# Kernel tuning notes

Measured on AMD Instinct MI355X. Metric: run time of the kernel, lower is better.

The kernel has to match this reference:

```python
import jax, jax.numpy as jnp
import numpy as np

B, S, D = 2, 2048, 2048
H, KV, HD = 32, 8, 64          # n_heads, n_kv_heads, head_dim
NREP = H // KV                 # GQA repeat factor
ROPE_THETA = 500000.0          # llama3 base


def setup_inputs() -> dict:
    key = jax.random.key(0)
    ks = jax.random.split(key, 5)
    scale = 1.0 / np.sqrt(D)
    x = jax.random.normal(ks[0], (B, S, D), dtype=jnp.float32)
    wq = jax.random.normal(ks[1], (D, H * HD), dtype=jnp.float32) * scale
    wk = jax.random.normal(ks[2], (D, KV * HD), dtype=jnp.float32) * scale
    wv = jax.random.normal(ks[3], (D, KV * HD), dtype=jnp.float32) * scale
    wo = jax.random.normal(ks[4], (H * HD, D), dtype=jnp.float32) * scale
    # real rotary freqs, matching precompute_freqs_cis: angle[t, j] = t / theta^(2j/HD)
    inv_freq = 1.0 / (ROPE_THETA ** (np.arange(0, HD, 2, dtype=np.float32) / HD))
    t = np.arange(S, dtype=np.float32)
    ang = np.outer(t, inv_freq)  # (S, HD//2)
    freqs_cos = jnp.asarray(np.cos(ang), dtype=jnp.float32)
    freqs_sin = jnp.asarray(np.sin(ang), dtype=jnp.float32)
    return {"x": x, "wq": wq, "wk": wk, "wv": wv, "wo": wo,
            "freqs_cos": freqs_cos, "freqs_sin": freqs_sin}


def _apply_rope(t, cos, sin):
    # t: (B, S, nh, HD); pairs (even, odd) = (real, imag) of complex number
    tr = t.reshape(*t.shape[:-1], HD // 2, 2)
    re, im = tr[..., 0], tr[..., 1]
    c = cos[None, :, None, :]   # (1, S, 1, HD//2)
    s = sin[None, :, None, :]
    out_re = re * c - im * s
    out_im = re * s + im * c
    return jnp.stack([out_re, out_im], axis=-1).reshape(t.shape)


def reference(x, wq, wk, wv, wo, freqs_cos, freqs_sin):
    bsz, seq_len, _ = x.shape
    xq = (x @ wq).reshape(bsz, seq_len, H, HD)
    xk = (x @ wk).reshape(bsz, seq_len, KV, HD)
    xv = (x @ wv).reshape(bsz, seq_len, KV, HD)
    xq = _apply_rope(xq, freqs_cos, freqs_sin)
    xk = _apply_rope(xk, freqs_cos, freqs_sin)
    # GQA without materializing repeated KV: group query heads by KV head
    q = xq.transpose(0, 2, 1, 3).reshape(bsz, KV, NREP, seq_len, HD)  # bgrqh
    k = xk.transpose(0, 2, 1, 3)                                      # bgkh over seq k
    v = xv.transpose(0, 2, 1, 3)
    scores = jnp.einsum("bgrqh,bgkh->bgrqk", q, k) / jnp.sqrt(jnp.float32(HD))
    causal = jnp.tril(jnp.ones((seq_len, seq_len), dtype=bool))
    scores = jnp.where(causal[None, None, None], scores, -jnp.inf)
    probs = jax.nn.softmax(scores.astype(jnp.float32), axis=-1).astype(q.dtype)
    out = jnp.einsum("bgrqk,bgkh->bgrqh", probs, v)
    out = out.reshape(bsz, H, seq_len, HD).transpose(0, 2, 1, 3).reshape(bsz, seq_len, H * HD)
    return out @ wo
```

## Files before the change

kernel.cpp:

```cpp
#include <hip/hip_runtime.h>
#include <hip/hip_bf16.h>

typedef __attribute__((ext_vector_type(8))) short bf16x8;
typedef __attribute__((ext_vector_type(4))) float f32x4;
typedef __attribute__((ext_vector_type(16))) float f32x16;

#define S_LEN 2048
#define DMODEL 2048
#define NH 32
#define NKV 8
#define HDIM 64
#define NQKV 3072
#define BROWS 4096
#define LOG2E 1.4426950408889634f

__device__ __forceinline__ float bf2f(unsigned short u) {
    union { unsigned int i; float f; } v; v.i = ((unsigned int)u) << 16; return v.f;
}
__device__ __forceinline__ unsigned short f2bf(float f) {
    union { float f; unsigned int i; } v; v.f = f;
    unsigned int r = v.i + 0x7fffu + ((v.i >> 16) & 1u);
    return (unsigned short)(r >> 16);
}

__device__ __forceinline__ unsigned cvtpk_bf16(float lo, float hi) {
    unsigned r;
    asm("v_cvt_pk_bf16_f32 %0, %1, %2" : "=v"(r) : "v"(lo), "v"(hi));
    return r;
}
__device__ __forceinline__ void pl32swap(unsigned &a, unsigned &b) {
    asm("v_permlane32_swap_b32 %0, %1" : "+v"(a), "+v"(b));
}
__device__ __forceinline__ float exp2_fast(float x) {
    float r;
    asm("v_exp_f32 %0, %1" : "=v"(r) : "v"(x));
    return r;
}

__device__ __forceinline__ void gload_lds16(const void* g, void* l) {
    __builtin_amdgcn_global_load_lds(
        (const __attribute__((address_space(1))) unsigned int*)(unsigned long long)g,
        (__attribute__((address_space(3))) unsigned int*)(unsigned int)(unsigned long long)l,
        16, 0, 0);
}

#define VMW(n) asm volatile("s_waitcnt vmcnt(" #n ")" ::: "memory")
#define CFENCE() asm volatile("" ::: "memory")

__global__ void cast_x_kernel(const float* __restrict__ x, unsigned short* __restrict__ xb) {
    int idx = blockIdx.x * blockDim.x + threadIdx.x;
    float4 v = ((const float4*)x)[idx];
    ushort4 o;
    o.x = f2bf(v.x); o.y = f2bf(v.y); o.z = f2bf(v.z); o.w = f2bf(v.w);
    ((ushort4*)xb)[idx] = o;
}

__global__ void tcast_kernel(const float* __restrict__ src, unsigned short* __restrict__ dst,
                             int K, int N) {
    __shared__ float t[32][33];
    int n0 = blockIdx.x * 32, k0 = blockIdx.y * 32;
    int tx = threadIdx.x & 31, ty = threadIdx.x >> 5;
#pragma unroll
    for (int i = 0; i < 32; i += 8)
        t[ty + i][tx] = src[(size_t)(k0 + ty + i) * N + n0 + tx];
    __syncthreads();
#pragma unroll
    for (int i = 0; i < 32; i += 8)
        dst[(size_t)(n0 + ty + i) * K + k0 + tx] = f2bf(t[tx][ty + i]);
}

__global__ void vtrans_kernel(const unsigned short* __restrict__ qkv,
                              unsigned short* __restrict__ vt) {
    __shared__ unsigned short t[32][33];
    int s0 = blockIdx.x * 32;
    int hd0 = (blockIdx.y & 1) * 32;
    int bg = blockIdx.y >> 1;
    int b = bg >> 3, g = bg & 7;
    int tx = threadIdx.x & 31, ty = threadIdx.x >> 5;
#pragma unroll
    for (int i = 0; i < 32; i += 8)
        t[ty + i][tx] = qkv[(size_t)(b * S_LEN + s0 + ty + i) * NQKV + 2560 + g * 64 + hd0 + tx];
    __syncthreads();
#pragma unroll
    for (int i = 0; i < 32; i += 8)
        vt[(size_t)(bg * 64 + hd0 + ty + i) * S_LEN + s0 + tx] = t[tx][ty + i];
}

template <int NJF, int OUTF32>
__global__ __launch_bounds__(512, 2) void gemm_deep_kernel(
    const unsigned short* __restrict__ A,
    const unsigned short* __restrict__ BT,
    void* __restrict__ Cv,
    int M, int N, int K, int nbx) {
    extern __shared__ __align__(16) unsigned short lds[];
    constexpr int BUFS = 4096 + NJF * 2048;
    constexpr int NBL = NJF / 2;

    const int nwg = gridDim.x;
    const int cpx = nwg >> 3;
    const int swz = ((int)blockIdx.x & 7) * cpx + ((int)blockIdx.x >> 3);
    const int m0 = (swz / nbx) * 128, n0 = (swz % nbx) * (NJF * 64);

    const int tid = threadIdx.x;
    const int lane = tid & 63, wid = tid >> 6;
    const int wr = wid >> 2, wc = wid & 3;
    const int l16 = lane & 15, lg = lane >> 4;

    const int sr = tid >> 2, sk = tid & 3;
    const int kc = (sk ^ ((sr >> 1) & 3)) * 8;
    const size_t K128 = (size_t)128 * K;
    const unsigned short* gA = A + (size_t)(m0 + sr) * K + kc;
    const unsigned short* gB = BT + (size_t)(n0 + sr) * K + kc;

#define DSTAGE(T) do { \
    const int _b = (T) & 3; \
    gload_lds16(gA + (size_t)(T) * 32, lds + _b * BUFS + tid * 8); \
    _Pragma("unroll") for (int j = 0; j < NBL; ++j) \
        gload_lds16(gB + (size_t)(T) * 32 + (size_t)j * K128, \
                    lds + _b * BUFS + 4096 + j * 4096 + tid * 8); \
} while (0)
#define VMW_3L() do { if constexpr (NJF == 6) { VMW(12); } else { VMW(9); } } while (0)
#define VMW_2L() do { if constexpr (NJF == 6) { VMW(8); } else { VMW(6); } } while (0)
#define VMW_1L() do { if constexpr (NJF == 6) { VMW(4); } else { VMW(3); } } while (0)

    f32x4 acc[4][NJF];
#pragma unroll
    for (int i = 0; i < 4; ++i)
#pragma unroll
        for (int j = 0; j < NJF; ++j)
#pragma unroll
            for (int e = 0; e < 4; ++e) acc[i][j][e] = 0.f;

    const int NT = K >> 5;
    DSTAGE(0); DSTAGE(1); DSTAGE(2);

    for (int t = 0; t < NT; ++t) {
        if (t + 3 < NT) { DSTAGE(t + 3); VMW_3L(); }
        else if (t + 2 < NT) { VMW_2L(); }
        else if (t + 1 < NT) { VMW_1L(); }
        else { VMW(0); }
        __builtin_amdgcn_s_barrier();
        CFENCE();

        const unsigned short* bufp = lds + (t & 3) * BUFS;
        bf16x8 af[4], bfv[NJF];
#pragma unroll
        for (int mi = 0; mi < 4; ++mi) {
            const int rA = wr * 64 + mi * 16 + l16;
            af[mi] = *(const bf16x8*)(bufp + rA * 32 + ((lg ^ ((rA >> 1) & 3)) * 8));
        }
#pragma unroll
        for (int nj = 0; nj < NJF; ++nj) {
            const int rB = nj * 64 + wc * 16 + l16;
            bfv[nj] = *(const bf16x8*)(bufp + 4096 + rB * 32 + ((lg ^ ((rB >> 1) & 3)) * 8));
        }
#pragma unroll
        for (int mi = 0; mi < 4; ++mi)
#pragma unroll
            for (int nj = 0; nj < NJF; ++nj)
                acc[mi][nj] = __builtin_amdgcn_mfma_f32_16x16x32_bf16(
                    af[mi], bfv[nj], acc[mi][nj], 0, 0, 0);
        CFENCE();
        __builtin_amdgcn_s_barrier();
        CFENCE();
    }

#pragma unroll
    for (int mi = 0; mi < 4; ++mi) {
        const int row = m0 + wr * 64 + mi * 16 + lg * 4;
#pragma unroll
        for (int e = 0; e < 4; ++e) {
            if (OUTF32) {
                float* Cf = (float*)Cv;
#pragma unroll
                for (int nj = 0; nj < NJF; ++nj)
                    Cf[(size_t)(row + e) * N + n0 + nj * 64 + wc * 16 + l16] = acc[mi][nj][e];
            } else {
                unsigned short* Cb = (unsigned short*)Cv;
#pragma unroll
                for (int nj = 0; nj < NJF; ++nj)
                    Cb[(size_t)(row + e) * N + n0 + nj * 64 + wc * 16 + l16] = f2bf(acc[mi][nj][e]);
            }
        }
    }
#undef DSTAGE
#undef VMW_3L
#undef VMW_2L
#undef VMW_1L
}

template <int OUTF32>
__global__ __launch_bounds__(256) void gemm_bt_kernel(
    const unsigned short* __restrict__ A,
    const unsigned short* __restrict__ BT,
    void* __restrict__ Cv,
    int M, int N, int K) {
    __shared__ __align__(16) unsigned short Als[128 * 32];
    __shared__ __align__(16) unsigned short Bls[128 * 32];

    const int tid = threadIdx.x;
    const int lane = tid & 63;
    const int wid = tid >> 6;
    const int wr = wid >> 1, wc = wid & 1;
    const int l16 = lane & 15, lg = lane >> 4;
    const int m0 = blockIdx.y * 128, n0 = blockIdx.x * 128;

    f32x4 acc[4][4];
#pragma unroll
    for (int i = 0; i < 4; ++i)
#pragma unroll
        for (int j = 0; j < 4; ++j)
#pragma unroll
            for (int e = 0; e < 4; ++e) acc[i][j][e] = 0.f;

    const int f0 = tid, f1 = 256 + tid;
    const int ar0 = f0 >> 2, ac0 = (f0 & 3) * 8;
    const int ar1 = f1 >> 2, ac1 = (f1 & 3) * 8;
    const size_t Abase = (size_t)m0 * K;
    const size_t Bbase = (size_t)n0 * K;

    for (int k0 = 0; k0 < K; k0 += 32) {
        __syncthreads();
        gload_lds16(A + Abase + (size_t)ar0 * K + k0 + ac0, Als + f0 * 8);
        gload_lds16(A + Abase + (size_t)ar1 * K + k0 + ac1, Als + f1 * 8);
        gload_lds16(BT + Bbase + (size_t)ar0 * K + k0 + ac0, Bls + f0 * 8);
        gload_lds16(BT + Bbase + (size_t)ar1 * K + k0 + ac1, Bls + f1 * 8);
        __syncthreads();
        bf16x8 af[4], bfv[4];
#pragma unroll
        for (int i = 0; i < 4; ++i)
            af[i] = *(const bf16x8*)(Als + (wr * 64 + i * 16 + l16) * 32 + lg * 8);
#pragma unroll
        for (int j = 0; j < 4; ++j)
            bfv[j] = *(const bf16x8*)(Bls + (wc * 64 + j * 16 + l16) * 32 + lg * 8);
#pragma unroll
        for (int i = 0; i < 4; ++i)
#pragma unroll
            for (int j = 0; j < 4; ++j)
                acc[i][j] = __builtin_amdgcn_mfma_f32_16x16x32_bf16(af[i], bfv[j], acc[i][j], 0, 0, 0);
    }

    const int row_base = m0 + wr * 64 + lg * 4;
    const int col_base = n0 + wc * 64 + l16;
    if (OUTF32) {
        float* Cf = (float*)Cv;
#pragma unroll
        for (int i = 0; i < 4; ++i)
#pragma unroll
            for (int r = 0; r < 4; ++r)
#pragma unroll
                for (int j = 0; j < 4; ++j)
                    Cf[(size_t)(row_base + i * 16 + r) * N + col_base + j * 16] = acc[i][j][r];
    } else {
        unsigned short* Cb = (unsigned short*)Cv;
#pragma unroll
        for (int i = 0; i < 4; ++i)
#pragma unroll
            for (int r = 0; r < 4; ++r)
#pragma unroll
                for (int j = 0; j < 4; ++j)
                    Cb[(size_t)(row_base + i * 16 + r) * N + col_base + j * 16] = f2bf(acc[i][j][r]);
    }
}

__global__ void rope_kernel(unsigned short* __restrict__ qkv,
                            const float* __restrict__ fc, const float* __restrict__ fs) {
    const int PAIRS = 1280;
    int idx = blockIdx.x * blockDim.x + threadIdx.x;
    int row = idx / PAIRS;
    int w = idx - row * PAIRS;
    int s = row & (S_LEN - 1);
    int col = (w < 1024) ? (w * 2) : (2048 + (w - 1024) * 2);
    int f = (col & 63) >> 1;
    float c = fc[s * 32 + f], sn = fs[s * 32 + f];
    unsigned int* p = (unsigned int*)(qkv + (size_t)row * NQKV + col);
    unsigned int v = *p;
    float re = bf2f((unsigned short)(v & 0xffffu));
    float im = bf2f((unsigned short)(v >> 16));
    float oro = re * c - im * sn;
    float oim = re * sn + im * c;
    if (w < 1024) { oro *= 0.125f * LOG2E; oim *= 0.125f * LOG2E; }
    *p = (unsigned int)f2bf(oro) | ((unsigned int)f2bf(oim) << 16);
}

__global__ __launch_bounds__(256) void attn_kernel(
    const unsigned short* __restrict__ qkv,
    const unsigned short* __restrict__ vt,
    unsigned short* __restrict__ aout) {
    __shared__ __align__(16) unsigned short Kls[2][64 * 64];
    __shared__ __align__(16) unsigned short Vls[2][64 * 64];
    __shared__ float Fbuf[4][32];

    const int tid = threadIdx.x, lane = tid & 63, wid = tid >> 6;
    const int l31 = lane & 31, hi = lane >> 5;
    const int g = blockIdx.x, b = blockIdx.y;
    const int h = g * 4 + wid;

    const int srow = tid >> 3, schk = tid & 7;
    const int sc = schk ^ (srow & 7);
    const unsigned short* kgs = qkv + (size_t)(b * S_LEN + srow) * NQKV + 2048 + g * 64 + sc * 8;
    const unsigned short* vgs = vt + (size_t)((b * 8 + g) * 64 + srow) * S_LEN + sc * 8;
    const int dd = tid * 8;

    const int xr = l31 & 7;

    const int chunk = 63 - (int)blockIdx.z;
    const int q0 = chunk * 32;
    const int ntiles = (chunk >> 1) + 1;
    const int qg_row = q0 + l31;

    bf16x8 qf[4];
    {
        const unsigned short* qp =
            qkv + (size_t)(b * S_LEN + q0 + l31) * NQKV + h * HDIM + hi * 8;
#pragma unroll
        for (int s = 0; s < 4; ++s) qf[s] = *(const bf16x8*)(qp + s * 16);
    }

    float l_r = 0.f;
    f32x16 oacc0, oacc1;
#pragma unroll
    for (int r = 0; r < 16; ++r) { oacc0[r] = 0.f; oacc1[r] = 0.f; }

    gload_lds16(kgs, Kls[0] + dd);
    gload_lds16(kgs + (size_t)32 * NQKV, Kls[0] + dd + 2048);
    gload_lds16(vgs, Vls[0] + dd);
    gload_lds16(vgs + (size_t)32 * S_LEN, Vls[0] + dd + 2048);
    __syncthreads();

    for (int t = 0; t < ntiles; ++t) {
        const int kv0 = t * 64;
        if (t + 1 < ntiles) {
            const int nkv = kv0 + 64;
            unsigned short* kd = Kls[(t + 1) & 1] + dd;
            unsigned short* vd = Vls[(t + 1) & 1] + dd;
            gload_lds16(kgs + (size_t)nkv * NQKV, kd);
            gload_lds16(kgs + (size_t)(nkv + 32) * NQKV, kd + 2048);
            gload_lds16(vgs + nkv, vd);
            gload_lds16(vgs + (size_t)32 * S_LEN + nkv, vd + 2048);
        }
        const unsigned short* Kb = Kls[t & 1];
        const unsigned short* Vb = Vls[t & 1];

        f32x16 s0, s1;
#pragma unroll
        for (int r = 0; r < 16; ++r) { s0[r] = 0.f; s1[r] = 0.f; }
        __builtin_amdgcn_s_setprio(1);
#pragma unroll
        for (int s = 0; s < 4; ++s) {
            const int coff = ((s * 2 + hi) ^ xr) * 8;
            bf16x8 kf0 = *(const bf16x8*)(Kb + l31 * 64 + coff);
            bf16x8 kf1 = *(const bf16x8*)(Kb + (32 + l31) * 64 + coff);
            s0 = __builtin_amdgcn_mfma_f32_32x32x16_bf16(kf0, qf[s], s0, 0, 0, 0);
            s1 = __builtin_amdgcn_mfma_f32_32x32x16_bf16(kf1, qf[s], s1, 0, 0, 0);
        }
        __builtin_amdgcn_s_setprio(0);
        if (t == ntiles - 1) {
#pragma unroll
            for (int r = 0; r < 16; ++r) {
                int kvr = kv0 + (r & 3) + 8 * (r >> 2) + 4 * hi;
                if (kvr > qg_row) s0[r] = -3.0e38f;
                if (kvr + 32 > qg_row) s1[r] = -3.0e38f;
            }
        }
        float r0 = 0.f, r1 = 0.f, r2 = 0.f, r3 = 0.f;
#pragma unroll
        for (int r = 0; r < 16; r += 4) {
            s0[r + 0] = exp2_fast(s0[r + 0]); r0 += s0[r + 0];
            s0[r + 1] = exp2_fast(s0[r + 1]); r1 += s0[r + 1];
            s0[r + 2] = exp2_fast(s0[r + 2]); r2 += s0[r + 2];
            s0[r + 3] = exp2_fast(s0[r + 3]); r3 += s0[r + 3];
        }
#pragma unroll
        for (int r = 0; r < 16; r += 4) {
            s1[r + 0] = exp2_fast(s1[r + 0]); r0 += s1[r + 0];
            s1[r + 1] = exp2_fast(s1[r + 1]); r1 += s1[r + 1];
            s1[r + 2] = exp2_fast(s1[r + 2]); r2 += s1[r + 2];
            s1[r + 3] = exp2_fast(s1[r + 3]); r3 += s1[r + 3];
        }
        l_r += (r0 + r1) + (r2 + r3);

        unsigned pw[4][4];
#define BUILD_PA(c, S, base)                                    \
        {                                                       \
            unsigned x0 = cvtpk_bf16(S[base + 0], S[base + 1]); \
            unsigned y0 = cvtpk_bf16(S[base + 4], S[base + 5]); \
            pl32swap(x0, y0);                                   \
            unsigned x1 = cvtpk_bf16(S[base + 2], S[base + 3]); \
            unsigned y1 = cvtpk_bf16(S[base + 6], S[base + 7]); \
            pl32swap(x1, y1);                                   \
            pw[c][0] = x0; pw[c][1] = x1; pw[c][2] = y0; pw[c][3] = y1; \
        }
        BUILD_PA(0, s0, 0)
        BUILD_PA(1, s0, 8)
        BUILD_PA(2, s1, 0)
        BUILD_PA(3, s1, 8)
#undef BUILD_PA

        __builtin_amdgcn_s_setprio(1);
#pragma unroll
        for (int c = 0; c < 4; ++c) {
            union { unsigned u[4]; bf16x8 v; } pa;
            pa.u[0] = pw[c][0]; pa.u[1] = pw[c][1]; pa.u[2] = pw[c][2]; pa.u[3] = pw[c][3];
            const int coff = ((c * 2 + hi) ^ xr) * 8;
            bf16x8 vf0 = *(const bf16x8*)(Vb + l31 * 64 + coff);
            bf16x8 vf1 = *(const bf16x8*)(Vb + (32 + l31) * 64 + coff);
            oacc0 = __builtin_amdgcn_mfma_f32_32x32x16_bf16(pa.v, vf0, oacc0, 0, 0, 0);
            oacc1 = __builtin_amdgcn_mfma_f32_32x32x16_bf16(pa.v, vf1, oacc1, 0, 0, 0);
        }
        __builtin_amdgcn_s_setprio(0);
        __syncthreads();
    }

    l_r += __shfl_xor(l_r, 32);
    if (lane < 32) Fbuf[wid][l31] = 1.0f / l_r;
    asm volatile("s_waitcnt lgkmcnt(0)" ::: "memory");
#pragma unroll
    for (int rg = 0; rg < 4; ++rg) {
#pragma unroll
        for (int rr = 0; rr < 4; ++rr) {
            int row = 8 * rg + 4 * hi + rr;
            float inv = Fbuf[wid][row];
            int r = rg * 4 + rr;
            size_t orow = (size_t)(b * S_LEN + q0 + row) * DMODEL + h * HDIM;
            aout[orow + l31] = f2bf(oacc0[r] * inv);
            aout[orow + 32 + l31] = f2bf(oacc1[r] * inv);
        }
    }
}

extern "C" void kernel_launch(void* const* d_in, const int* in_sizes, int n_in,
                              void* d_out, int out_size, void* d_ws, size_t ws_size,
                              hipStream_t stream) {
    const float* x = (const float*)d_in[0];
    const float* wq = (const float*)d_in[1];
    const float* wk = (const float*)d_in[2];
    const float* wv = (const float*)d_in[3];
    const float* wo = (const float*)d_in[4];
    const float* fc = (const float*)d_in[5];
    const float* fs = (const float*)d_in[6];
    float* out = (float*)d_out;

    unsigned short* xb = (unsigned short*)d_ws;
    unsigned short* wqkvT = xb + (size_t)BROWS * DMODEL;
    unsigned short* woT = wqkvT + (size_t)NQKV * DMODEL;
    unsigned short* qkvb = woT + (size_t)DMODEL * DMODEL;
    unsigned short* aoutb = xb;
    unsigned short* vtb = wqkvT;

    hipError_t e1 = hipFuncSetAttribute(
        reinterpret_cast<const void*>(&gemm_deep_kernel<6, 0>),
        hipFuncAttributeMaxDynamicSharedMemorySize, 131072);
    hipError_t e2 = hipFuncSetAttribute(
        reinterpret_cast<const void*>(&gemm_deep_kernel<4, 1>),
        hipFuncAttributeMaxDynamicSharedMemorySize, 98304);
    const bool big = (e1 == hipSuccess && e2 == hipSuccess);

    cast_x_kernel<<<(BROWS * DMODEL / 4) / 256, 256, 0, stream>>>(x, xb);
    tcast_kernel<<<dim3(DMODEL / 32, DMODEL / 32), 256, 0, stream>>>(wq, wqkvT, DMODEL, DMODEL);
    tcast_kernel<<<dim3(512 / 32, DMODEL / 32), 256, 0, stream>>>(wk, wqkvT + (size_t)2048 * DMODEL, DMODEL, 512);
    tcast_kernel<<<dim3(512 / 32, DMODEL / 32), 256, 0, stream>>>(wv, wqkvT + (size_t)2560 * DMODEL, DMODEL, 512);
    tcast_kernel<<<dim3(DMODEL / 32, DMODEL / 32), 256, 0, stream>>>(wo, woT, DMODEL, DMODEL);
    if (big)
        gemm_deep_kernel<6, 0><<<(BROWS / 128) * (NQKV / 384), 512, 131072, stream>>>(
            xb, wqkvT, qkvb, BROWS, NQKV, DMODEL, NQKV / 384);
    else
        gemm_bt_kernel<0><<<dim3(NQKV / 128, BROWS / 128), 256, 0, stream>>>(
            xb, wqkvT, qkvb, BROWS, NQKV, DMODEL);
    rope_kernel<<<(BROWS * 1280) / 256, 256, 0, stream>>>(qkvb, fc, fs);
    vtrans_kernel<<<dim3(S_LEN / 32, 32), 256, 0, stream>>>(qkvb, vtb);
    attn_kernel<<<dim3(NKV, 2, 64), 256, 0, stream>>>(qkvb, vtb, aoutb);
    if (big)
        gemm_deep_kernel<4, 1><<<(BROWS / 128) * (DMODEL / 256), 512, 98304, stream>>>(
            aoutb, woT, out, BROWS, DMODEL, DMODEL, DMODEL / 256);
    else
        gemm_bt_kernel<1><<<dim3(DMODEL / 128, BROWS / 128), 256, 0, stream>>>(
            aoutb, woT, out, BROWS, DMODEL, DMODEL);
}
```

Measured before the change: 184.6 us.

## Fuse RoPE into QKV GEMM epilogue with register-resident B operand

Replaces the deep LDS-staged QKV GEMM plus separate RoPE kernel with a new GEMM that stages only A through a triple-buffered LDS ring and loads B fragments straight from global into registers, ping-ponging two register sets. RoPE rotation and the Q scaling are applied in the epilogue using a lane shuffle to pair even and odd columns, which removes a full read-modify-write pass over the QKV buffer and one launch. It also adds an lgkmcnt wait before barriers in the existing deep GEMM. Risks include higher register pressure, uncoalesced B loads from global, and a smaller 128x192 tile with 256 threads.

```diff
diff --git a/kernel.cpp b/kernel.cpp
--- a/kernel.cpp
+++ b/kernel.cpp
@@ -45,7 +45,9 @@
 }
 
 #define VMW(n) asm volatile("s_waitcnt vmcnt(" #n ")" ::: "memory")
+#define LGW()  asm volatile("s_waitcnt lgkmcnt(0)" ::: "memory")
 #define CFENCE() asm volatile("" ::: "memory")
+#define READS_DONE_FENCE() do { LGW(); __builtin_amdgcn_sched_barrier(0); } while (0)
 
 __global__ void cast_x_kernel(const float* __restrict__ x, unsigned short* __restrict__ xb) {
     int idx = blockIdx.x * blockDim.x + threadIdx.x;
@@ -84,6 +86,122 @@
 #pragma unroll
     for (int i = 0; i < 32; i += 8)
         vt[(size_t)(bg * 64 + hd0 + ty + i) * S_LEN + s0 + tx] = t[tx][ty + i];
+}
+
+__global__ __launch_bounds__(256, 2) void gemm_qkv_breg(
+    const unsigned short* __restrict__ A,
+    const unsigned short* __restrict__ BT,
+    unsigned short* __restrict__ C,
+    const float* __restrict__ fc, const float* __restrict__ fs,
+    int M, int N, int K, int nbx) {
+    __shared__ __align__(16) unsigned short Als[3][128 * 32];
+
+    const int nwg = gridDim.x;
+    const int cpx = nwg >> 3;
+    const int swz = ((int)blockIdx.x & 7) * cpx + ((int)blockIdx.x >> 3);
+    const int m0 = (swz / nbx) * 128, n0 = (swz % nbx) * 192;
+
+    const int tid = threadIdx.x;
+    const int lane = tid & 63, wid = tid >> 6;
+    const int wr = wid >> 1, wc = wid & 1;
+    const int l16 = lane & 15, lg = lane >> 4;
+
+    const int r0 = tid >> 2, sk0 = tid & 3;
+    const int kc0 = (sk0 ^ ((r0 >> 1) & 3)) * 8;
+    const int r1 = r0 + 64;
+    const int kc1 = (sk0 ^ ((r1 >> 1) & 3)) * 8;
+    const unsigned short* gA0 = A + (size_t)(m0 + r0) * K + kc0;
+    const unsigned short* gA1 = A + (size_t)(m0 + r1) * K + kc1;
+
+#define ASTAGE(T) do { const int _b = (T) % 3; \
+    gload_lds16(gA0 + (size_t)(T) * 32, &Als[_b][tid * 8]); \
+    gload_lds16(gA1 + (size_t)(T) * 32, &Als[_b][2048 + tid * 8]); } while (0)
+
+    const unsigned short* gBp = BT + (size_t)(n0 + wc * 16 + l16) * K + lg * 8;
+#define LOADB(DST, T) do { \
+    _Pragma("unroll") for (int nj = 0; nj < 6; ++nj) \
+        DST[nj] = *(const bf16x8*)(gBp + (size_t)nj * 32 * K + (size_t)(T) * 32); } while (0)
+
+    f32x4 acc[4][6];
+#pragma unroll
+    for (int i = 0; i < 4; ++i)
+#pragma unroll
+        for (int j = 0; j < 6; ++j)
+#pragma unroll
+            for (int e = 0; e < 4; ++e) acc[i][j][e] = 0.f;
+
+    bf16x8 bA[6], bB[6];
+
+#define COMPUTE(T, BB) do { \
+    const unsigned short* _bp = &Als[(T) % 3][0]; \
+    bf16x8 _af[4]; \
+    _Pragma("unroll") for (int mi = 0; mi < 4; ++mi) { \
+        const int rA = wr * 64 + mi * 16 + l16; \
+        _af[mi] = *(const bf16x8*)(_bp + rA * 32 + ((lg ^ ((rA >> 1) & 3)) * 8)); \
+    } \
+    _Pragma("unroll") for (int mi = 0; mi < 4; ++mi) \
+        _Pragma("unroll") for (int nj = 0; nj < 6; ++nj) \
+            acc[mi][nj] = __builtin_amdgcn_mfma_f32_16x16x32_bf16( \
+                _af[mi], BB[nj], acc[mi][nj], 0, 0, 0); \
+} while (0)
+
+    const int NT = K >> 5;
+    ASTAGE(0);
+    LOADB(bA, 0);
+    ASTAGE(1);
+
+    for (int t = 0; t < NT; t += 2) {
+        READS_DONE_FENCE();
+        VMW(2);
+        __builtin_amdgcn_s_barrier();
+        CFENCE();
+        LOADB(bB, t + 1);
+        if (t + 2 < NT) ASTAGE(t + 2);
+        COMPUTE(t, bA);
+        READS_DONE_FENCE();
+        if (t + 2 < NT) { VMW(2); } else { VMW(0); }
+        __builtin_amdgcn_s_barrier();
+        CFENCE();
+        if (t + 2 < NT) LOADB(bA, t + 2);
+        if (t + 3 < NT) ASTAGE(t + 3);
+        COMPUTE(t + 1, bB);
+    }
+
+    const int cb0 = n0 + wc * 16;
+    const float QS = 0.125f * LOG2E;
+    const int fe = wc * 8 + (l16 >> 1);
+    const int fo = 16 + fe;
+    const bool evenl = !(l16 & 1);
+#pragma unroll
+    for (int mi = 0; mi < 4; ++mi) {
+        const int rowb = m0 + wr * 64 + mi * 16 + lg * 4;
+#pragma unroll
+        for (int e = 0; e < 4; ++e) {
+            const int row = rowb + e;
+            const int seq = row & (S_LEN - 1);
+            const float cA = fc[seq * 32 + fe], sA = fs[seq * 32 + fe];
+            const float cB = fc[seq * 32 + fo], sB = fs[seq * 32 + fo];
+#pragma unroll
+            for (int nj = 0; nj < 6; ++nj) {
+                const int cbase = cb0 + nj * 32;
+                float v = acc[mi][nj][e];
+                float o;
+                if (cbase >= 2560) {
+                    o = v;
+                } else {
+                    float p = __shfl_xor(v, 1);
+                    float cc = (nj & 1) ? cB : cA;
+                    float ss = (nj & 1) ? sB : sA;
+                    o = fmaf(v, cc, evenl ? -(p * ss) : (p * ss));
+                    if (cbase < 2048) o *= QS;
+                }
+                C[(size_t)row * N + cbase + l16] = f2bf(o);
+            }
+        }
+    }
+#undef ASTAGE
+#undef LOADB
+#undef COMPUTE
 }
 
 template <int NJF, int OUTF32>
@@ -161,6 +279,7 @@
                 acc[mi][nj] = __builtin_amdgcn_mfma_f32_16x16x32_bf16(
                     af[mi], bfv[nj], acc[mi][nj], 0, 0, 0);
         CFENCE();
+        READS_DONE_FENCE();
         __builtin_amdgcn_s_barrier();
         CFENCE();
     }
@@ -261,26 +380,6 @@
                 for (int j = 0; j < 4; ++j)
                     Cb[(size_t)(row_base + i * 16 + r) * N + col_base + j * 16] = f2bf(acc[i][j][r]);
     }
-}
-
-__global__ void rope_kernel(unsigned short* __restrict__ qkv,
-                            const float* __restrict__ fc, const float* __restrict__ fs) {
-    const int PAIRS = 1280;
-    int idx = blockIdx.x * blockDim.x + threadIdx.x;
-    int row = idx / PAIRS;
-    int w = idx - row * PAIRS;
-    int s = row & (S_LEN - 1);
-    int col = (w < 1024) ? (w * 2) : (2048 + (w - 1024) * 2);
-    int f = (col & 63) >> 1;
-    float c = fc[s * 32 + f], sn = fs[s * 32 + f];
-    unsigned int* p = (unsigned int*)(qkv + (size_t)row * NQKV + col);
-    unsigned int v = *p;
-    float re = bf2f((unsigned short)(v & 0xffffu));
-    float im = bf2f((unsigned short)(v >> 16));
-    float oro = re * c - im * sn;
-    float oim = re * sn + im * c;
-    if (w < 1024) { oro *= 0.125f * LOG2E; oim *= 0.125f * LOG2E; }
-    *p = (unsigned int)f2bf(oro) | ((unsigned int)f2bf(oim) << 16);
 }
 
 __global__ __launch_bounds__(256) void attn_kernel(
@@ -448,26 +547,18 @@
     unsigned short* aoutb = xb;
     unsigned short* vtb = wqkvT;
 
-    hipError_t e1 = hipFuncSetAttribute(
-        reinterpret_cast<const void*>(&gemm_deep_kernel<6, 0>),
-        hipFuncAttributeMaxDynamicSharedMemorySize, 131072);
     hipError_t e2 = hipFuncSetAttribute(
         reinterpret_cast<const void*>(&gemm_deep_kernel<4, 1>),
         hipFuncAttributeMaxDynamicSharedMemorySize, 98304);
-    const bool big = (e1 == hipSuccess && e2 == hipSuccess);
+    const bool big = (e2 == hipSuccess);
 
     cast_x_kernel<<<(BROWS * DMODEL / 4) / 256, 256, 0, stream>>>(x, xb);
     tcast_kernel<<<dim3(DMODEL / 32, DMODEL / 32), 256, 0, stream>>>(wq, wqkvT, DMODEL, DMODEL);
     tcast_kernel<<<dim3(512 / 32, DMODEL / 32), 256, 0, stream>>>(wk, wqkvT + (size_t)2048 * DMODEL, DMODEL, 512);
     tcast_kernel<<<dim3(512 / 32, DMODEL / 32), 256, 0, stream>>>(wv, wqkvT + (size_t)2560 * DMODEL, DMODEL, 512);
     tcast_kernel<<<dim3(DMODEL / 32, DMODEL / 32), 256, 0, stream>>>(wo, woT, DMODEL, DMODEL);
-    if (big)
-        gemm_deep_kernel<6, 0><<<(BROWS / 128) * (NQKV / 384), 512, 131072, stream>>>(
-            xb, wqkvT, qkvb, BROWS, NQKV, DMODEL, NQKV / 384);
-    else
-        gemm_bt_kernel<0><<<dim3(NQKV / 128, BROWS / 128), 256, 0, stream>>>(
-            xb, wqkvT, qkvb, BROWS, NQKV, DMODEL);
-    rope_kernel<<<(BROWS * 1280) / 256, 256, 0, stream>>>(qkvb, fc, fs);
+    gemm_qkv_breg<<<(BROWS / 128) * (NQKV / 192), 256, 0, stream>>>(
+        xb, wqkvT, qkvb, fc, fs, BROWS, NQKV, DMODEL, NQKV / 192);
     vtrans_kernel<<<dim3(S_LEN / 32, 32), 256, 0, stream>>>(qkvb, vtb);
     attn_kernel<<<dim3(NKV, 2, 64), 256, 0, stream>>>(qkvb, vtb, aoutb);
     if (big)
```

Result: slower. 232.6 us (+26.0%).
